# Performance work log

Measured on AMD Instinct MI355X. Metric: run time of the kernel, lower is better.

The kernel has to match this reference:

```python
import jax, jax.numpy as jnp
import numpy as np
import math

H = 1024   # d_model
N = 64     # d_state
L_LEN = 1024
DT_MIN, DT_MAX = 1e-3, 1e-1


def setup_inputs() -> dict:
    key = jax.random.key(0)
    k1, k2, k3, k4, k5, k6 = jax.random.split(key, 6)
    log_dt = jnp.linspace(math.log(DT_MIN), math.log(DT_MAX), H).astype(jnp.float32)
    # negative real parts so Lambda_bar^l stays bounded for l up to L (stable S4D init)
    Lambda_re = -jnp.abs(jax.random.normal(k1, (H, N), jnp.float32)) * 0.5 - 0.1
    Lambda_im = jax.random.normal(k2, (H, N), jnp.float32) * math.pi
    B = jax.random.normal(k3, (H, N, 1), jnp.float32)
    C_re = jax.random.normal(k4, (H, 1, N), jnp.float32)
    C_im = jax.random.normal(k5, (H, 1, N), jnp.float32)
    D = jax.random.normal(k6, (H,), jnp.float32)
    return {
        "log_dt": log_dt,
        "Lambda_re": Lambda_re,
        "Lambda_im": Lambda_im,
        "B": B,
        "C_re": C_re,
        "C_im": C_im,
        "D": D,
        "L": L_LEN,
    }


def reference(log_dt, Lambda_re, Lambda_im, B, C_re, C_im, D, L):
    dt = jnp.exp(log_dt)                                 # (H,)
    Lam = Lambda_re + 1j * Lambda_im                     # (H,N) complex64
    dtA = dt[:, None] * Lam                              # (H,N)
    Lambda_bar_minus1 = jnp.expm1(dtA)                   # exp(dtA) - 1, same math, stabler
    B_bar = Lambda_bar_minus1 / Lam * B[:, :, 0]         # (H,N)
    C = C_re[:, 0, :] + 1j * C_im[:, 0, :]               # (H,N)
    CB = C * B_bar                                       # (H,N)
    l = jnp.arange(L)
    # Lambda_bar**l == exp(dtA * l): log-space Vandermonde, (H,N,L)
    V = jnp.exp(dtA[:, :, None] * l)
    K = jnp.einsum('hn,hnl->hl', CB, V)                  # (H,L) complex
    K = 2.0 * K.real
    K = K + D[:, None] * (l == 0).astype(K.dtype)
    return K
```

## Files before the change

### kernel.cpp

```cpp
#include <hip/hip_runtime.h>
#include <math.h>


#define NSTATE 64
#define TCHUNK 4

__global__ __launch_bounds__(256) void ssk_diag_kernel(
    const float* __restrict__ log_dt,
    const float* __restrict__ Lre,
    const float* __restrict__ Lim,
    const float* __restrict__ Bv,
    const float* __restrict__ Cre,
    const float* __restrict__ Cim,
    const float* __restrict__ Dv,
    float* __restrict__ K,
    int L)
{
    const int h   = blockIdx.x;
    const int tid = threadIdx.x;

    __shared__ float2 s_a[NSTATE];
    __shared__ float2 s_step[NSTATE];
    __shared__ float2 s_cb[NSTATE];

    if (tid < NSTATE) {
        const int n   = tid;
        const int idx = h * NSTATE + n;
        const float dt  = expf(log_dt[h]);
        const float lre = Lre[idx];
        const float lim = Lim[idx];
        const float are = dt * lre;
        const float aim = dt * lim;

        float sy, cy;
        sincosf(aim, &sy, &cy);
        const float sh    = sinf(0.5f * aim);
        const float em_re = expm1f(are) * cy - 2.0f * sh * sh;
        const float em_im = expf(are) * sy;

        const float inv_d = 1.0f / (lre * lre + lim * lim);
        const float b     = Bv[idx];
        const float bb_re = (em_re * lre + em_im * lim) * inv_d * b;
        const float bb_im = (em_im * lre - em_re * lim) * inv_d * b;

        const float cre = Cre[idx];
        const float cim = Cim[idx];
        s_cb[n]   = make_float2(cre * bb_re - cim * bb_im,
                                cre * bb_im + cim * bb_re);
        s_a[n]    = make_float2(are, aim);
        s_step[n] = make_float2(em_re + 1.0f, em_im);
    }
    __syncthreads();

    const float Dh = Dv[h];

    for (int l0 = tid * TCHUNK; l0 < L; l0 += blockDim.x * TCHUNK) {
        const float fl = (float)l0;
        float acc[TCHUNK];
        #pragma unroll
        for (int t = 0; t < TCHUNK; ++t) acc[t] = 0.0f;

        #pragma unroll 4
        for (int n = 0; n < NSTATE; ++n) {
            const float2 a  = s_a[n];
            const float2 st = s_step[n];
            const float2 cb = s_cb[n];

            const float mag = __expf(a.x * fl);
            float s, c;
            __sincosf(a.y * fl, &s, &c);
            float wr = mag * (cb.x * c - cb.y * s);
            float wi = mag * (cb.x * s + cb.y * c);

            #pragma unroll
            for (int t = 0; t < TCHUNK; ++t) {
                acc[t] += wr;
                if (t < TCHUNK - 1) {
                    const float nr = wr * st.x - wi * st.y;
                    wi = wr * st.y + wi * st.x;
                    wr = nr;
                }
            }
        }

        float4 outv;
        outv.x = 2.0f * acc[0];
        outv.y = 2.0f * acc[1];
        outv.z = 2.0f * acc[2];
        outv.w = 2.0f * acc[3];
        if (l0 == 0) outv.x += Dh;
        *(float4*)(K + h * L + l0) = outv;
    }
}

extern "C" void kernel_launch(void* const* d_in, const int* in_sizes, int n_in,
                              void* d_out, int out_size, void* d_ws, size_t ws_size,
                              hipStream_t stream) {
    const float* log_dt = (const float*)d_in[0];
    const float* Lre    = (const float*)d_in[1];
    const float* Lim    = (const float*)d_in[2];
    const float* B      = (const float*)d_in[3];
    const float* Cre    = (const float*)d_in[4];
    const float* Cim    = (const float*)d_in[5];
    const float* D      = (const float*)d_in[6];
    const int H = in_sizes[0];
    const int L = out_size / H;
    float* K = (float*)d_out;

    ssk_diag_kernel<<<H, 256, 0, stream>>>(log_dt, Lre, Lim, B, Cre, Cim, D, K, L);
}
```

Baseline: 83.80 us.

## Pack state pairs into float2 vector math and double per-thread time chunk

Moves the shared state arrays from array-of-structs to struct-of-arrays so two states load as one vector, and runs the complex recurrence on two states at once with ext_vector_type float2, which can map to packed FP32 instructions on CDNA. TCHUNK goes from 4 to 8 and block size from 256 to 128, so each thread computes eight outputs per exp/sincos seed, halving the transcendental cost per output. The tradeoff is more registers, fewer threads per block, and a longer recurrence chain, which may cost some accuracy.

```diff
diff --git a/kernel.cpp b/kernel.cpp
--- a/kernel.cpp
+++ b/kernel.cpp
@@ -3,9 +3,11 @@
 
 
 #define NSTATE 64
-#define TCHUNK 4
+#define TCHUNK 8
 
-__global__ __launch_bounds__(256) void ssk_diag_kernel(
+typedef float v2f __attribute__((ext_vector_type(2)));
+
+__global__ __launch_bounds__(128) void ssk_diag_kernel(
     const float* __restrict__ log_dt,
     const float* __restrict__ Lre,
     const float* __restrict__ Lim,
@@ -19,9 +21,9 @@
     const int h   = blockIdx.x;
     const int tid = threadIdx.x;
 
-    __shared__ float2 s_a[NSTATE];
-    __shared__ float2 s_step[NSTATE];
-    __shared__ float2 s_cb[NSTATE];
+    __shared__ float s_are[NSTATE], s_aim[NSTATE];
+    __shared__ float s_str[NSTATE], s_sti[NSTATE];
+    __shared__ float s_cbr[NSTATE], s_cbi[NSTATE];
 
     if (tid < NSTATE) {
         const int n   = tid;
@@ -45,10 +47,12 @@
 
         const float cre = Cre[idx];
         const float cim = Cim[idx];
-        s_cb[n]   = make_float2(cre * bb_re - cim * bb_im,
-                                cre * bb_im + cim * bb_re);
-        s_a[n]    = make_float2(are, aim);
-        s_step[n] = make_float2(em_re + 1.0f, em_im);
+        s_cbr[n] = cre * bb_re - cim * bb_im;
+        s_cbi[n] = cre * bb_im + cim * bb_re;
+        s_are[n] = are;
+        s_aim[n] = aim;
+        s_str[n] = em_re + 1.0f;
+        s_sti[n] = em_im;
     }
     __syncthreads();
 
@@ -56,40 +60,55 @@
 
     for (int l0 = tid * TCHUNK; l0 < L; l0 += blockDim.x * TCHUNK) {
         const float fl = (float)l0;
-        float acc[TCHUNK];
+        v2f acc[TCHUNK];
         #pragma unroll
-        for (int t = 0; t < TCHUNK; ++t) acc[t] = 0.0f;
+        for (int t = 0; t < TCHUNK; ++t) acc[t] = (v2f){0.0f, 0.0f};
 
-        #pragma unroll 4
-        for (int n = 0; n < NSTATE; ++n) {
-            const float2 a  = s_a[n];
-            const float2 st = s_step[n];
-            const float2 cb = s_cb[n];
+        #pragma unroll 2
+        for (int n = 0; n < NSTATE; n += 2) {
+            const v2f ar  = *(const v2f*)&s_are[n];
+            const v2f ai  = *(const v2f*)&s_aim[n];
+            const v2f str_= *(const v2f*)&s_str[n];
+            const v2f sti = *(const v2f*)&s_sti[n];
+            const v2f cbr = *(const v2f*)&s_cbr[n];
+            const v2f cbi = *(const v2f*)&s_cbi[n];
 
-            const float mag = __expf(a.x * fl);
-            float s, c;
-            __sincosf(a.y * fl, &s, &c);
-            float wr = mag * (cb.x * c - cb.y * s);
-            float wi = mag * (cb.x * s + cb.y * c);
+            const v2f argr = ar * fl;
+            const v2f argi = ai * fl;
+            const float m0 = __expf(argr.x);
+            const float m1 = __expf(argr.y);
+            float s0, c0, s1, c1;
+            __sincosf(argi.x, &s0, &c0);
+            __sincosf(argi.y, &s1, &c1);
+            const v2f zr = {m0 * c0, m1 * c1};
+            const v2f zi = {m0 * s0, m1 * s1};
+
+            v2f wr = cbr * zr - cbi * zi;
+            v2f wi = cbr * zi + cbi * zr;
 
             #pragma unroll
             for (int t = 0; t < TCHUNK; ++t) {
                 acc[t] += wr;
                 if (t < TCHUNK - 1) {
-                    const float nr = wr * st.x - wi * st.y;
-                    wi = wr * st.y + wi * st.x;
+                    const v2f nr = wr * str_ - wi * sti;
+                    wi = wr * sti + wi * str_;
                     wr = nr;
                 }
             }
         }
 
-        float4 outv;
-        outv.x = 2.0f * acc[0];
-        outv.y = 2.0f * acc[1];
-        outv.z = 2.0f * acc[2];
-        outv.w = 2.0f * acc[3];
-        if (l0 == 0) outv.x += Dh;
-        *(float4*)(K + h * L + l0) = outv;
+        float4 o0, o1;
+        o0.x = 2.0f * (acc[0].x + acc[0].y);
+        o0.y = 2.0f * (acc[1].x + acc[1].y);
+        o0.z = 2.0f * (acc[2].x + acc[2].y);
+        o0.w = 2.0f * (acc[3].x + acc[3].y);
+        o1.x = 2.0f * (acc[4].x + acc[4].y);
+        o1.y = 2.0f * (acc[5].x + acc[5].y);
+        o1.z = 2.0f * (acc[6].x + acc[6].y);
+        o1.w = 2.0f * (acc[7].x + acc[7].y);
+        if (l0 == 0) o0.x += Dh;
+        *(float4*)(K + h * L + l0)     = o0;
+        *(float4*)(K + h * L + l0 + 4) = o1;
     }
 }
 
@@ -107,5 +126,5 @@
     const int L = out_size / H;
     float* K = (float*)d_out;
 
-    ssk_diag_kernel<<<H, 256, 0, stream>>>(log_dt, Lre, Lim, B, Cre, Cim, D, K, L);
+    ssk_diag_kernel<<<H, 128, 0, stream>>>(log_dt, Lre, Lim, B, Cre, Cim, D, K, L);
 }
```

Result: faster. 77.48 us (-7.5%).
